# Optimization experiments

Hardware: AMD Instinct MI355X
Metric: run time of the kernel (lower is better)

The kernel has to match this reference:

```python
import jax, jax.numpy as jnp
import numpy as np


def _conv_valid(x, w):
    # x: [B, Cin, H, W], w: [Cout, Cin, K, K], stride 1, no padding
    return jax.lax.conv_general_dilated(
        x, w, window_strides=(1, 1), padding='VALID',
        dimension_numbers=('NCHW', 'OIHW', 'NCHW'))


def _buggy_maxpool(x, k=2):
    # Faithful to the source MaxPool: window of size kxk slides with STRIDE 1,
    # but only the first H//k x W//k positions are kept (top-left region).
    nh = x.shape[2] // k
    nw = x.shape[3] // k
    m = jax.lax.reduce_window(
        x, -jnp.inf, jax.lax.max,
        window_dimensions=(1, 1, k, k),
        window_strides=(1, 1, 1, 1),
        padding='VALID')  # [B, C, H-k+1, W-k+1]
    return m[:, :, :nh, :nw]


def setup_inputs() -> dict:
    key = jax.random.key(0)
    ks = jax.random.split(key, 9)
    B = 8192
    x = jax.random.normal(ks[0], (B, 3, 32, 32), dtype=jnp.float32)
    s = 0.1
    conv1_w = jax.random.normal(ks[1], (6, 3, 5, 5), dtype=jnp.float32) * s
    conv2_w = jax.random.normal(ks[2], (16, 6, 5, 5), dtype=jnp.float32) * s
    fc1_w = jax.random.normal(ks[3], (120, 400), dtype=jnp.float32) * s
    fc1_b = jax.random.normal(ks[4], (120,), dtype=jnp.float32) * s
    fc2_w = jax.random.normal(ks[5], (84, 120), dtype=jnp.float32) * s
    fc2_b = jax.random.normal(ks[6], (84,), dtype=jnp.float32) * s
    fc3_w = jax.random.normal(ks[7], (10, 84), dtype=jnp.float32) * s
    fc3_b = jax.random.normal(ks[8], (10,), dtype=jnp.float32) * s
    return {
        'x': x,
        'conv1_w': conv1_w, 'conv2_w': conv2_w,
        'fc1_w': fc1_w, 'fc1_b': fc1_b,
        'fc2_w': fc2_w, 'fc2_b': fc2_b,
        'fc3_w': fc3_w, 'fc3_b': fc3_b,
    }


def reference(x, conv1_w, conv2_w, fc1_w, fc1_b, fc2_w, fc2_b, fc3_w, fc3_b):
    h = _buggy_maxpool(jax.nn.relu(_conv_valid(x, conv1_w)))   # [B,6,14,14]
    h = _buggy_maxpool(jax.nn.relu(_conv_valid(h, conv2_w)))   # [B,16,5,5]
    h = h.reshape(-1, 16 * 5 * 5)                              # [B,400]
    h = jax.nn.relu(h @ fc1_w.T + fc1_b)                       # [B,120]
    h = jax.nn.relu(h @ fc2_w.T + fc2_b)                       # [B,84]
    return h @ fc3_w.T + fc3_b                                 # [B,10]
```

## Files before the change

### kernel.cpp

```cpp
#include <hip/hip_runtime.h>


typedef float v2f __attribute__((ext_vector_type(2)));
__device__ __forceinline__ v2f mk2(float a, float b) { v2f t; t.x = a; t.y = b; return t; }
__device__ __forceinline__ v2f shfl2(v2f v, int src) {
    v2f r; r.x = __shfl(v.x, src, 64); r.y = __shfl(v.y, src, 64); return r;
}

constexpr int THREADS = 512;
constexpr int IPB = 8;

constexpr int W1P_OFF = 0;
constexpr int W2P_OFF = 540;
constexpr int IMG_BASE = 2940;
constexpr int XS_OFF = 0;
constexpr int P1_OFF = 0;
constexpr int P2_OFF = 0;
constexpr int F1_OFF = 0;
constexpr int F2_OFF = 128;
constexpr int IMG_STRIDE = 900;
constexpr int LDS_FLOATS = IMG_BASE + IPB * IMG_STRIDE;

__device__ __forceinline__ void wave_sync() {
    asm volatile("s_waitcnt lgkmcnt(0)" ::: "memory");
}

extern "C" __global__ __launch_bounds__(THREADS, 8)
void lenet_fused(const float* __restrict__ x,
                 const float* __restrict__ w1,
                 const float* __restrict__ w2,
                 const float* __restrict__ fc1w, const float* __restrict__ fc1b,
                 const float* __restrict__ fc2w, const float* __restrict__ fc2b,
                 const float* __restrict__ fc3w, const float* __restrict__ fc3b,
                 float* __restrict__ out)
{
    __shared__ __align__(16) float lds[LDS_FLOATS];
    const int tid  = threadIdx.x;
    const int lane = tid & 63;
    const int wv   = tid >> 6;
    const int img0 = blockIdx.x * IPB;
    const v2f zero2 = mk2(0.f, 0.f);

    for (int i = tid; i < 540; i += THREADS) {
        int ocp = i / 180, rem = i - ocp * 180;
        int ii = rem / 12, kh = rem - ii * 12, kc = kh >> 1, h = kh & 1;
        lds[W1P_OFF + i] = (kc < 5) ? w1[(2 * ocp + h) * 75 + ii * 5 + kc] : 0.f;
    }
    for (int i = tid; i < 2400; i += THREADS) {
        int ocp = i / 300, rem = i - ocp * 300, k = rem >> 1, h = rem & 1;
        lds[W2P_OFF + i] = w2[(2 * ocp + h) * 150 + k];
    }

    float* base = lds + IMG_BASE + wv * IMG_STRIDE;
    {
        const float4* xg = (const float4*)(x + (size_t)(img0 + wv) * 3072);
        float4* d = (float4*)(base + XS_OFF);
        for (int i = lane; i < 180; i += 64) {
            int c = i / 60, rem = i - c * 60;
            int r = rem >> 2, c4 = rem & 3;
            d[c * 75 + r * 5 + c4] = xg[c * 256 + r * 8 + c4];
        }
    }
    __syncthreads();

    float* p1 = base + P1_OFF;

    {
        const int l   = (lane < 33) ? lane : 32;
        const int ocp = l / 11;
        const int r   = l - ocp * 11;
        const float4* xs = (const float4*)(base + XS_OFF);

        v2f acc[11];
        #pragma unroll
        for (int c = 0; c < 11; ++c) acc[c] = zero2;

        #pragma unroll
        for (int i = 0; i < 15; ++i) {
            const int ci = i / 5, kr = i - ci * 5;
            const int b = ci * 75 + (r + kr) * 5;
            float4 A0 = xs[b], A1 = xs[b + 1], A2 = xs[b + 2], A3 = xs[b + 3];
            const float* w1f = lds + W1P_OFF + ocp * 180 + i * 12;
            float4 q0 = *(const float4*)(w1f);
            float4 q1 = *(const float4*)(w1f + 4);
            float2 q2 = *(const float2*)(w1f + 8);
            v2f W[5];
            W[0] = mk2(q0.x, q0.y); W[1] = mk2(q0.z, q0.w);
            W[2] = mk2(q1.x, q1.y); W[3] = mk2(q1.z, q1.w);
            W[4] = mk2(q2.x, q2.y);
            float xa[16];
            xa[0]=A0.x; xa[1]=A0.y; xa[2]=A0.z;  xa[3]=A0.w;
            xa[4]=A1.x; xa[5]=A1.y; xa[6]=A1.z;  xa[7]=A1.w;
            xa[8]=A2.x; xa[9]=A2.y; xa[10]=A2.z; xa[11]=A2.w;
            xa[12]=A3.x; xa[13]=A3.y; xa[14]=A3.z; xa[15]=A3.w;
            #pragma unroll
            for (int kc = 0; kc < 5; ++kc) {
                #pragma unroll
                for (int c = 0; c < 11; ++c) {
                    acc[c] = __builtin_elementwise_fma(
                        mk2(xa[c + kc], xa[c + kc]), W[kc], acc[c]);
                }
            }
        }

        v2f pm[10], m[10];
        #pragma unroll
        for (int c = 0; c < 10; ++c) {
            v2f a0 = __builtin_elementwise_max(acc[c], zero2);
            v2f a1 = __builtin_elementwise_max(acc[c + 1], zero2);
            pm[c] = __builtin_elementwise_max(a0, a1);
        }
        #pragma unroll
        for (int c = 0; c < 10; ++c)
            m[c] = __builtin_elementwise_max(pm[c], shfl2(pm[c], lane + 1));
        wave_sync();
        if (r < 10) {
            const int oc0 = ocp * 2;
            float* d0 = p1 + oc0 * 120 + r * 12;
            float* d1 = p1 + (oc0 + 1) * 120 + r * 12;
            *(float4*)(d0)     = make_float4(m[0].x, m[1].x, m[2].x, m[3].x);
            *(float4*)(d0 + 4) = make_float4(m[4].x, m[5].x, m[6].x, m[7].x);
            *(float2*)(d0 + 8) = make_float2(m[8].x, m[9].x);
            *(float4*)(d1)     = make_float4(m[0].y, m[1].y, m[2].y, m[3].y);
            *(float4*)(d1 + 4) = make_float4(m[4].y, m[5].y, m[6].y, m[7].y);
            *(float2*)(d1 + 8) = make_float2(m[8].y, m[9].y);
        }
    }
    wave_sync();

    float* p2 = base + P2_OFF;
    {
        const int l   = (lane < 48) ? lane : 47;
        const int ocp = l / 6;
        const int r   = l - ocp * 6;
        const float4* pa4 = (const float4*)p1;
        const float2* pa2 = (const float2*)p1;

        v2f acc[6];
        #pragma unroll
        for (int c = 0; c < 6; ++c) acc[c] = zero2;

        #pragma unroll
        for (int i = 0; i < 30; ++i) {
            const int ci = i / 5, kr = i - ci * 5;
            float4 A0 = pa4[ci * 30 + (r + kr) * 3 + 0];
            float4 A1 = pa4[ci * 30 + (r + kr) * 3 + 1];
            float2 A2 = pa2[ci * 60 + (r + kr) * 6 + 4];
            const float* w2f = lds + W2P_OFF + ocp * 300 + i * 10;
            v2f W[5];
            if ((i & 1) == 0) {
                float4 q0 = *(const float4*)(w2f);
                float4 q1 = *(const float4*)(w2f + 4);
                float2 q2 = *(const float2*)(w2f + 8);
                W[0] = mk2(q0.x, q0.y); W[1] = mk2(q0.z, q0.w);
                W[2] = mk2(q1.x, q1.y); W[3] = mk2(q1.z, q1.w);
                W[4] = mk2(q2.x, q2.y);
            } else {
                float2 r0 = *(const float2*)(w2f);
                float4 r1 = *(const float4*)(w2f + 2);
                float2 r2 = *(const float2*)(w2f + 6);
                float2 r3 = *(const float2*)(w2f + 8);
                W[0] = mk2(r0.x, r0.y); W[1] = mk2(r1.x, r1.y);
                W[2] = mk2(r1.z, r1.w); W[3] = mk2(r2.x, r2.y);
                W[4] = mk2(r3.x, r3.y);
            }
            float xa[10];
            xa[0]=A0.x; xa[1]=A0.y; xa[2]=A0.z; xa[3]=A0.w;
            xa[4]=A1.x; xa[5]=A1.y; xa[6]=A1.z; xa[7]=A1.w;
            xa[8]=A2.x; xa[9]=A2.y;
            #pragma unroll
            for (int kc = 0; kc < 5; ++kc) {
                #pragma unroll
                for (int c = 0; c < 6; ++c) {
                    acc[c] = __builtin_elementwise_fma(
                        mk2(xa[c + kc], xa[c + kc]), W[kc], acc[c]);
                }
            }
        }

        v2f pm[5], m[5];
        #pragma unroll
        for (int c = 0; c < 5; ++c) {
            v2f a0 = __builtin_elementwise_max(acc[c], zero2);
            v2f a1 = __builtin_elementwise_max(acc[c + 1], zero2);
            pm[c] = __builtin_elementwise_max(a0, a1);
        }
        #pragma unroll
        for (int c = 0; c < 5; ++c)
            m[c] = __builtin_elementwise_max(pm[c], shfl2(pm[c], lane + 1));
        wave_sync();
        if (r < 5) {
            const int oc0 = ocp * 2;
            #pragma unroll
            for (int c = 0; c < 5; ++c) {
                p2[oc0 * 25 + r * 5 + c]       = m[c].x;
                p2[(oc0 + 1) * 25 + r * 5 + c] = m[c].y;
            }
        }
    }
    __syncthreads();

    float* scr = lds;
    if (tid < 480) {
        const int row  = tid >> 2;
        const int rh   = tid & 3;
        const int half = rh >> 1;
        const int imh  = rh & 1;
        const float4* wrow = (const float4*)(fc1w + row * 400) + half * 50;
        v2f acc[4];
        #pragma unroll
        for (int q = 0; q < 4; ++q) acc[q] = zero2;
        #pragma unroll 2
        for (int k = 0; k < 50; ++k) {
            float4 w4 = wrow[k];
            const v2f wxy = mk2(w4.x, w4.y), wzw = mk2(w4.z, w4.w);
            #pragma unroll
            for (int q = 0; q < 4; ++q) {
                const float4* ap = (const float4*)(lds + IMG_BASE + (imh * 4 + q) * IMG_STRIDE + P2_OFF) + half * 50;
                float4 a = ap[k];
                acc[q] = __builtin_elementwise_fma(mk2(a.x, a.y), wxy, acc[q]);
                acc[q] = __builtin_elementwise_fma(mk2(a.z, a.w), wzw, acc[q]);
            }
        }
        #pragma unroll
        for (int q = 0; q < 4; ++q)
            scr[(imh * 4 + q) * 240 + row * 2 + half] = acc[q].x + acc[q].y;
    }
    __syncthreads();

    if (tid < 120) {
        const float b = fc1b[tid];
        #pragma unroll
        for (int im = 0; im < 8; ++im) {
            float v = scr[im * 240 + tid * 2] + scr[im * 240 + tid * 2 + 1] + b;
            lds[IMG_BASE + im * IMG_STRIDE + F1_OFF + tid] = fmaxf(v, 0.f);
        }
    }
    __syncthreads();

    if (tid < 168) {
        const int row = tid >> 1;
        const int imh = tid & 1;
        const float4* wrow = (const float4*)(fc2w + row * 120);
        const float bz = fc2b[row];
        v2f acc[4];
        #pragma unroll
        for (int q = 0; q < 4; ++q) acc[q] = zero2;
        #pragma unroll 2
        for (int k = 0; k < 30; ++k) {
            float4 w4 = wrow[k];
            const v2f wxy = mk2(w4.x, w4.y), wzw = mk2(w4.z, w4.w);
            #pragma unroll
            for (int q = 0; q < 4; ++q) {
                const float4* fp = (const float4*)(lds + IMG_BASE + (imh * 4 + q) * IMG_STRIDE + F1_OFF);
                float4 a = fp[k];
                acc[q] = __builtin_elementwise_fma(mk2(a.x, a.y), wxy, acc[q]);
                acc[q] = __builtin_elementwise_fma(mk2(a.z, a.w), wzw, acc[q]);
            }
        }
        #pragma unroll
        for (int q = 0; q < 4; ++q)
            lds[IMG_BASE + (imh * 4 + q) * IMG_STRIDE + F2_OFF + row] =
                fmaxf(acc[q].x + acc[q].y + bz, 0.f);
    }
    __syncthreads();

    if (tid < 80) {
        const int im  = tid / 10;
        const int row = tid - im * 10;
        const float4* wrow = (const float4*)(fc3w + row * 84);
        const float4* f2 = (const float4*)(lds + IMG_BASE + im * IMG_STRIDE + F2_OFF);
        v2f acc = zero2;
        #pragma unroll
        for (int k = 0; k < 21; ++k) {
            float4 w4 = wrow[k];
            float4 a = f2[k];
            acc = __builtin_elementwise_fma(mk2(a.x, a.y), mk2(w4.x, w4.y), acc);
            acc = __builtin_elementwise_fma(mk2(a.z, a.w), mk2(w4.z, w4.w), acc);
        }
        out[(size_t)(img0 + im) * 10 + row] = acc.x + acc.y + fc3b[row];
    }
}

extern "C" void kernel_launch(void* const* d_in, const int* in_sizes, int n_in,
                              void* d_out, int out_size, void* d_ws, size_t ws_size,
                              hipStream_t stream) {
    const float* x    = (const float*)d_in[0];
    const float* w1   = (const float*)d_in[1];
    const float* w2   = (const float*)d_in[2];
    const float* fc1w = (const float*)d_in[3];
    const float* fc1b = (const float*)d_in[4];
    const float* fc2w = (const float*)d_in[5];
    const float* fc2b = (const float*)d_in[6];
    const float* fc3w = (const float*)d_in[7];
    const float* fc3b = (const float*)d_in[8];
    float* out = (float*)d_out;

    const int B = in_sizes[0] / 3072;
    const int grid = B / IPB;
    lenet_fused<<<grid, THREADS, 0, stream>>>(x, w1, w2, fc1w, fc1b,
                                              fc2w, fc2b, fc3w, fc3b, out);
}
```

Before: 211.2 us.

## Repack conv work across waves and register-block FC1/FC2 over rows and images

New measurement: 207.6 us. No clear change (-1.7%).

```diff
diff --git a/kernel.cpp b/kernel.cpp
--- a/kernel.cpp
+++ b/kernel.cpp
@@ -20,10 +20,7 @@
 constexpr int F2_OFF = 128;
 constexpr int IMG_STRIDE = 900;
 constexpr int LDS_FLOATS = IMG_BASE + IPB * IMG_STRIDE;
-
-__device__ __forceinline__ void wave_sync() {
-    asm volatile("s_waitcnt lgkmcnt(0)" ::: "memory");
-}
+constexpr int SCR_STRIDE = 242;
 
 extern "C" __global__ __launch_bounds__(THREADS, 8)
 void lenet_fused(const float* __restrict__ x,
@@ -51,8 +48,8 @@
         lds[W2P_OFF + i] = w2[(2 * ocp + h) * 150 + k];
     }
 
-    float* base = lds + IMG_BASE + wv * IMG_STRIDE;
     {
+        float* base = lds + IMG_BASE + wv * IMG_STRIDE;
         const float4* xg = (const float4*)(x + (size_t)(img0 + wv) * 3072);
         float4* d = (float4*)(base + XS_OFF);
         for (int i = lane; i < 180; i += 64) {
@@ -63,13 +60,18 @@
     }
     __syncthreads();
 
-    float* p1 = base + P1_OFF;
-
-    {
-        const int l   = (lane < 33) ? lane : 32;
-        const int ocp = l / 11;
-        const int r   = l - ocp * 11;
-        const float4* xs = (const float4*)(base + XS_OFF);
+    v2f m1[10];
+    int c1_store = 0;
+    float *c1_d0 = nullptr, *c1_d1 = nullptr;
+    if (wv < 5) {
+        const int l   = (lane < 55) ? lane : 54;
+        const int g   = l / 11;
+        const int r   = l - g * 11;
+        const int gid = wv * 5 + g;
+        const int gidc = (gid < 24) ? gid : 23;
+        const int img = gidc / 3;
+        const int ocp = gidc - img * 3;
+        const float4* xs = (const float4*)(lds + IMG_BASE + img * IMG_STRIDE + XS_OFF);
 
         v2f acc[11];
         #pragma unroll
@@ -103,7 +105,7 @@
             }
         }
 
-        v2f pm[10], m[10];
+        v2f pm[10];
         #pragma unroll
         for (int c = 0; c < 10; ++c) {
             v2f a0 = __builtin_elementwise_max(acc[c], zero2);
@@ -112,29 +114,38 @@
         }
         #pragma unroll
         for (int c = 0; c < 10; ++c)
-            m[c] = __builtin_elementwise_max(pm[c], shfl2(pm[c], lane + 1));
-        wave_sync();
-        if (r < 10) {
-            const int oc0 = ocp * 2;
-            float* d0 = p1 + oc0 * 120 + r * 12;
-            float* d1 = p1 + (oc0 + 1) * 120 + r * 12;
-            *(float4*)(d0)     = make_float4(m[0].x, m[1].x, m[2].x, m[3].x);
-            *(float4*)(d0 + 4) = make_float4(m[4].x, m[5].x, m[6].x, m[7].x);
-            *(float2*)(d0 + 8) = make_float2(m[8].x, m[9].x);
-            *(float4*)(d1)     = make_float4(m[0].y, m[1].y, m[2].y, m[3].y);
-            *(float4*)(d1 + 4) = make_float4(m[4].y, m[5].y, m[6].y, m[7].y);
-            *(float2*)(d1 + 8) = make_float2(m[8].y, m[9].y);
-        }
-    }
-    wave_sync();
-
-    float* p2 = base + P2_OFF;
-    {
-        const int l   = (lane < 48) ? lane : 47;
-        const int ocp = l / 6;
-        const int r   = l - ocp * 6;
-        const float4* pa4 = (const float4*)p1;
-        const float2* pa2 = (const float2*)p1;
+            m1[c] = __builtin_elementwise_max(pm[c], shfl2(pm[c], lane + 1));
+        c1_store = (gid < 24) && (r < 10);
+        float* p1 = lds + IMG_BASE + img * IMG_STRIDE + P1_OFF;
+        c1_d0 = p1 + (ocp * 2) * 120 + r * 12;
+        c1_d1 = c1_d0 + 120;
+    }
+    __syncthreads();
+    if (c1_store) {
+        *(float4*)(c1_d0)     = make_float4(m1[0].x, m1[1].x, m1[2].x, m1[3].x);
+        *(float4*)(c1_d0 + 4) = make_float4(m1[4].x, m1[5].x, m1[6].x, m1[7].x);
+        *(float2*)(c1_d0 + 8) = make_float2(m1[8].x, m1[9].x);
+        *(float4*)(c1_d1)     = make_float4(m1[0].y, m1[1].y, m1[2].y, m1[3].y);
+        *(float4*)(c1_d1 + 4) = make_float4(m1[4].y, m1[5].y, m1[6].y, m1[7].y);
+        *(float2*)(c1_d1 + 8) = make_float2(m1[8].y, m1[9].y);
+    }
+    __syncthreads();
+
+    v2f m2[5];
+    int c2_store = 0;
+    float* c2_p2 = nullptr;
+    int c2_oc0 = 0, c2_r = 0;
+    if (wv < 7) {
+        const int l    = (lane < 60) ? lane : 59;
+        const int g    = l / 6;
+        const int r    = l - g * 6;
+        const int gid2 = wv * 10 + g;
+        const int gc   = (gid2 < 64) ? gid2 : 63;
+        const int img  = gc >> 3;
+        const int ocp  = gc & 7;
+        const float* p1b = lds + IMG_BASE + img * IMG_STRIDE + P1_OFF;
+        const float4* pa4 = (const float4*)p1b;
+        const float2* pa2 = (const float2*)p1b;
 
         v2f acc[6];
         #pragma unroll
@@ -178,7 +189,7 @@
             }
         }
 
-        v2f pm[5], m[5];
+        v2f pm[5];
         #pragma unroll
         for (int c = 0; c < 5; ++c) {
             v2f a0 = __builtin_elementwise_max(acc[c], zero2);
@@ -187,44 +198,56 @@
         }
         #pragma unroll
         for (int c = 0; c < 5; ++c)
-            m[c] = __builtin_elementwise_max(pm[c], shfl2(pm[c], lane + 1));
-        wave_sync();
-        if (r < 5) {
-            const int oc0 = ocp * 2;
-            #pragma unroll
-            for (int c = 0; c < 5; ++c) {
-                p2[oc0 * 25 + r * 5 + c]       = m[c].x;
-                p2[(oc0 + 1) * 25 + r * 5 + c] = m[c].y;
-            }
+            m2[c] = __builtin_elementwise_max(pm[c], shfl2(pm[c], lane + 1));
+        c2_store = (gid2 < 64) && (r < 5);
+        c2_p2 = lds + IMG_BASE + img * IMG_STRIDE + P2_OFF;
+        c2_oc0 = ocp * 2;
+        c2_r = r;
+    }
+    __syncthreads();
+    if (c2_store) {
+        #pragma unroll
+        for (int c = 0; c < 5; ++c) {
+            c2_p2[c2_oc0 * 25 + c2_r * 5 + c]       = m2[c].x;
+            c2_p2[(c2_oc0 + 1) * 25 + c2_r * 5 + c] = m2[c].y;
         }
     }
     __syncthreads();
 
     float* scr = lds;
     if (tid < 480) {
-        const int row  = tid >> 2;
-        const int rh   = tid & 3;
-        const int half = rh >> 1;
-        const int imh  = rh & 1;
-        const float4* wrow = (const float4*)(fc1w + row * 400) + half * 50;
-        v2f acc[4];
-        #pragma unroll
-        for (int q = 0; q < 4; ++q) acc[q] = zero2;
+        const int rowq = tid >> 3;
+        const int half = (tid >> 2) & 1;
+        const int imh  = tid & 3;
+        const int i0 = imh * 2, i1 = i0 + 1;
+        const float4* ap0 = (const float4*)(lds + IMG_BASE + i0 * IMG_STRIDE + P2_OFF) + half * 50;
+        const float4* ap1 = (const float4*)(lds + IMG_BASE + i1 * IMG_STRIDE + P2_OFF) + half * 50;
+        const float* wb0 = fc1w + (rowq * 2) * 400 + half * 200;
+        const float* wb1 = wb0 + 400;
+        v2f a00 = zero2, a01 = zero2, a10 = zero2, a11 = zero2;
         #pragma unroll 2
-        for (int k = 0; k < 50; ++k) {
-            float4 w4 = wrow[k];
-            const v2f wxy = mk2(w4.x, w4.y), wzw = mk2(w4.z, w4.w);
-            #pragma unroll
-            for (int q = 0; q < 4; ++q) {
-                const float4* ap = (const float4*)(lds + IMG_BASE + (imh * 4 + q) * IMG_STRIDE + P2_OFF) + half * 50;
-                float4 a = ap[k];
-                acc[q] = __builtin_elementwise_fma(mk2(a.x, a.y), wxy, acc[q]);
-                acc[q] = __builtin_elementwise_fma(mk2(a.z, a.w), wzw, acc[q]);
-            }
-        }
-        #pragma unroll
-        for (int q = 0; q < 4; ++q)
-            scr[(imh * 4 + q) * 240 + row * 2 + half] = acc[q].x + acc[q].y;
+        for (int j = 0; j < 50; ++j) {
+            float4 a0 = ap0[j], a1 = ap1[j];
+            float4 w0 = *(const float4*)(wb0 + j * 4);
+            float4 w1_ = *(const float4*)(wb1 + j * 4);
+            const v2f a0xy = mk2(a0.x, a0.y), a0zw = mk2(a0.z, a0.w);
+            const v2f a1xy = mk2(a1.x, a1.y), a1zw = mk2(a1.z, a1.w);
+            const v2f w0xy = mk2(w0.x, w0.y), w0zw = mk2(w0.z, w0.w);
+            const v2f w1xy = mk2(w1_.x, w1_.y), w1zw = mk2(w1_.z, w1_.w);
+            a00 = __builtin_elementwise_fma(a0xy, w0xy, a00);
+            a00 = __builtin_elementwise_fma(a0zw, w0zw, a00);
+            a01 = __builtin_elementwise_fma(a1xy, w0xy, a01);
+            a01 = __builtin_elementwise_fma(a1zw, w0zw, a01);
+            a10 = __builtin_elementwise_fma(a0xy, w1xy, a10);
+            a10 = __builtin_elementwise_fma(a0zw, w1zw, a10);
+            a11 = __builtin_elementwise_fma(a1xy, w1xy, a11);
+            a11 = __builtin_elementwise_fma(a1zw, w1zw, a11);
+        }
+        const int r0 = rowq * 2, r1 = r0 + 1;
+        scr[i0 * SCR_STRIDE + r0 * 2 + half] = a00.x + a00.y;
+        scr[i1 * SCR_STRIDE + r0 * 2 + half] = a01.x + a01.y;
+        scr[i0 * SCR_STRIDE + r1 * 2 + half] = a10.x + a10.y;
+        scr[i1 * SCR_STRIDE + r1 * 2 + half] = a11.x + a11.y;
     }
     __syncthreads();
 
@@ -232,36 +255,45 @@
         const float b = fc1b[tid];
         #pragma unroll
         for (int im = 0; im < 8; ++im) {
-            float v = scr[im * 240 + tid * 2] + scr[im * 240 + tid * 2 + 1] + b;
-            lds[IMG_BASE + im * IMG_STRIDE + F1_OFF + tid] = fmaxf(v, 0.f);
+            float2 p = *(const float2*)(scr + im * SCR_STRIDE + tid * 2);
+            lds[IMG_BASE + im * IMG_STRIDE + F1_OFF + tid] = fmaxf(p.x + p.y + b, 0.f);
         }
     }
     __syncthreads();
 
     if (tid < 168) {
-        const int row = tid >> 1;
-        const int imh = tid & 1;
-        const float4* wrow = (const float4*)(fc2w + row * 120);
-        const float bz = fc2b[row];
-        v2f acc[4];
-        #pragma unroll
-        for (int q = 0; q < 4; ++q) acc[q] = zero2;
+        const int rowq = tid >> 2;
+        const int imh  = tid & 3;
+        const int i0 = imh * 2, i1 = i0 + 1;
+        const float4* fp0 = (const float4*)(lds + IMG_BASE + i0 * IMG_STRIDE + F1_OFF);
+        const float4* fp1 = (const float4*)(lds + IMG_BASE + i1 * IMG_STRIDE + F1_OFF);
+        const float* wb0 = fc2w + (rowq * 2) * 120;
+        const float* wb1 = wb0 + 120;
+        v2f a00 = zero2, a01 = zero2, a10 = zero2, a11 = zero2;
         #pragma unroll 2
-        for (int k = 0; k < 30; ++k) {
-            float4 w4 = wrow[k];
-            const v2f wxy = mk2(w4.x, w4.y), wzw = mk2(w4.z, w4.w);
-            #pragma unroll
-            for (int q = 0; q < 4; ++q) {
-                const float4* fp = (const float4*)(lds + IMG_BASE + (imh * 4 + q) * IMG_STRIDE + F1_OFF);
-                float4 a = fp[k];
-                acc[q] = __builtin_elementwise_fma(mk2(a.x, a.y), wxy, acc[q]);
-                acc[q] = __builtin_elementwise_fma(mk2(a.z, a.w), wzw, acc[q]);
-            }
-        }
-        #pragma unroll
-        for (int q = 0; q < 4; ++q)
-            lds[IMG_BASE + (imh * 4 + q) * IMG_STRIDE + F2_OFF + row] =
-                fmaxf(acc[q].x + acc[q].y + bz, 0.f);
+        for (int j = 0; j < 30; ++j) {
+            float4 a0 = fp0[j], a1 = fp1[j];
+            float4 w0 = *(const float4*)(wb0 + j * 4);
+            float4 w1_ = *(const float4*)(wb1 + j * 4);
+            const v2f a0xy = mk2(a0.x, a0.y), a0zw = mk2(a0.z, a0.w);
+            const v2f a1xy = mk2(a1.x, a1.y), a1zw = mk2(a1.z, a1.w);
+            const v2f w0xy = mk2(w0.x, w0.y), w0zw = mk2(w0.z, w0.w);
+            const v2f w1xy = mk2(w1_.x, w1_.y), w1zw = mk2(w1_.z, w1_.w);
+            a00 = __builtin_elementwise_fma(a0xy, w0xy, a00);
+            a00 = __builtin_elementwise_fma(a0zw, w0zw, a00);
+            a01 = __builtin_elementwise_fma(a1xy, w0xy, a01);
+            a01 = __builtin_elementwise_fma(a1zw, w0zw, a01);
+            a10 = __builtin_elementwise_fma(a0xy, w1xy, a10);
+            a10 = __builtin_elementwise_fma(a0zw, w1zw, a10);
+            a11 = __builtin_elementwise_fma(a1xy, w1xy, a11);
+            a11 = __builtin_elementwise_fma(a1zw, w1zw, a11);
+        }
+        const int r0 = rowq * 2, r1 = r0 + 1;
+        const float b0 = fc2b[r0], b1 = fc2b[r1];
+        lds[IMG_BASE + i0 * IMG_STRIDE + F2_OFF + r0] = fmaxf(a00.x + a00.y + b0, 0.f);
+        lds[IMG_BASE + i1 * IMG_STRIDE + F2_OFF + r0] = fmaxf(a01.x + a01.y + b0, 0.f);
+        lds[IMG_BASE + i0 * IMG_STRIDE + F2_OFF + r1] = fmaxf(a10.x + a10.y + b1, 0.f);
+        lds[IMG_BASE + i1 * IMG_STRIDE + F2_OFF + r1] = fmaxf(a11.x + a11.y + b1, 0.f);
     }
     __syncthreads();
 
```
